# Performance work log

Measured on AMD Instinct MI355X. Metric: run time of the kernel, lower is better.

The kernel has to match this reference:

```python
import jax, jax.numpy as jnp
import numpy as np

EMBED_DIM = 1024
NUM_MEMORY_SLOTS = 256
B, Q = 8, 4096


def setup_inputs() -> dict:
    key = jax.random.key(0)
    ks = jax.random.split(key, 6)
    s = 1.0 / np.sqrt(EMBED_DIM)
    return {
        "x": jax.random.normal(ks[0], (B, Q, EMBED_DIM), dtype=jnp.float32),
        "memory_bank": jax.random.normal(ks[1], (NUM_MEMORY_SLOTS, EMBED_DIM), dtype=jnp.float32),
        "Wq": jax.random.uniform(ks[2], (EMBED_DIM, EMBED_DIM), jnp.float32, -s, s),
        "bq": jax.random.uniform(ks[3], (EMBED_DIM,), jnp.float32, -s, s),
        "Wo": jax.random.uniform(ks[4], (EMBED_DIM, EMBED_DIM), jnp.float32, -s, s),
        "bo": jax.random.uniform(ks[5], (EMBED_DIM,), jnp.float32, -s, s),
    }


def reference(x, memory_bank, Wq, bq, Wo, bo):
    # query projection: [B,Q,E]
    queries = jnp.einsum('bqe,fe->bqf', x, Wq) + bq
    # attention over fixed memory bank: scores [B,Q,M]
    scores = jnp.einsum('bqe,me->bqm', queries, memory_bank)
    weights = jax.nn.softmax(scores, axis=-1)
    attended = jnp.einsum('bqm,me->bqe', weights, memory_bank)
    # output projection + residual
    return jnp.einsum('bqe,fe->bqf', attended, Wo) + bo + x
```

## Files before the change

### kernel.cpp

```cpp
#include <hip/hip_runtime.h>
#include <hip/hip_bf16.h>
#include <stdint.h>

#define TOK 32768
#define EMB 1024
#define MSL 256

typedef __attribute__((ext_vector_type(8))) short short8;
typedef __attribute__((ext_vector_type(4))) float f32x4;

__device__ __forceinline__ ushort f2bf(float f) {
    union { float f; uint32_t u; } c; c.f = f;
    uint32_t u = c.u;
    return (ushort)((u + 0x7fffu + ((u >> 16) & 1u)) >> 16);
}

__device__ __forceinline__ void split2(float f, ushort& h, ushort& l) {
    union { float f; uint32_t u; } c; c.f = f;
    h = (ushort)(c.u >> 16);
    union { uint32_t u; float f; } hv; hv.u = c.u & 0xffff0000u;
    union { float f; uint32_t u; } lc; lc.f = f - hv.f;
    l = (ushort)(lc.u >> 16);
}

__device__ __forceinline__ void async_copy16(const void* gsrc, void* ldst) {
    __builtin_amdgcn_global_load_lds(
        (const __attribute__((address_space(1))) uint32_t*)gsrc,
        (__attribute__((address_space(3))) uint32_t*)ldst,
        16, 0, 0);
}

__global__ __launch_bounds__(256) void split_f32(const float* __restrict__ in,
                                                 ushort* __restrict__ hi,
                                                 ushort* __restrict__ lo) {
    int i = blockIdx.x * 256 + threadIdx.x;
    float4 v = ((const float4*)in)[i];
    ushort4 h4, l4;
    split2(v.x, h4.x, l4.x); split2(v.y, h4.y, l4.y);
    split2(v.z, h4.z, l4.z); split2(v.w, h4.w, l4.w);
    ((ushort4*)hi)[i] = h4;
    ((ushort4*)lo)[i] = l4;
}

__global__ __launch_bounds__(256) void transpose_split(const float* __restrict__ in,
                                                       ushort* __restrict__ outh,
                                                       ushort* __restrict__ outl) {
    __shared__ float ld[64 * 65];
    const int t = threadIdx.x;
    const int eBase = blockIdx.x * 64;
    const int fBase = blockIdx.y * 64;
    #pragma unroll
    for (int r = 0; r < 16; ++r) {
        int row = r * 4 + (t >> 6);
        int col = t & 63;
        ld[row * 65 + col] = in[(size_t)(fBase + row) * EMB + eBase + col];
    }
    __syncthreads();
    #pragma unroll
    for (int r = 0; r < 16; ++r) {
        int row = r * 4 + (t >> 6);
        int col = t & 63;
        float v = ld[col * 65 + row];
        ushort h, l; split2(v, h, l);
        size_t o = (size_t)(eBase + row) * EMB + fBase + col;
        outh[o] = h; outl[o] = l;
    }
}

__global__ __launch_bounds__(256) void dot_c(const float* __restrict__ bq,
                                             const float* __restrict__ mb,
                                             float* __restrict__ c) {
    int m = blockIdx.x * 4 + (threadIdx.x >> 6);
    int lane = threadIdx.x & 63;
    const float4* mrow = (const float4*)(mb + (size_t)m * EMB);
    const float4* brow = (const float4*)bq;
    float s = 0.f;
    #pragma unroll
    for (int k = 0; k < 4; ++k) {
        float4 a = mrow[lane + k * 64];
        float4 b = brow[lane + k * 64];
        s += a.x * b.x + a.y * b.y + a.z * b.z + a.w * b.w;
    }
    #pragma unroll
    for (int off = 32; off; off >>= 1) s += __shfl_xor(s, off, 64);
    if (lane == 0) c[m] = s;
}

__global__ __launch_bounds__(256) void softmax_rows(const float* __restrict__ scores,
                                                    ushort* __restrict__ w) {
    int row = blockIdx.x * 4 + (threadIdx.x >> 6);
    int lane = threadIdx.x & 63;
    const float4 v = ((const float4*)(scores + (size_t)row * MSL))[lane];
    float mx = fmaxf(fmaxf(v.x, v.y), fmaxf(v.z, v.w));
    #pragma unroll
    for (int off = 32; off; off >>= 1) mx = fmaxf(mx, __shfl_xor(mx, off, 64));
    float e0 = __expf(v.x - mx), e1 = __expf(v.y - mx);
    float e2 = __expf(v.z - mx), e3 = __expf(v.w - mx);
    float s = e0 + e1 + e2 + e3;
    #pragma unroll
    for (int off = 32; off; off >>= 1) s += __shfl_xor(s, off, 64);
    float inv = 1.0f / s;
    ushort4 o;
    o.x = f2bf(e0 * inv); o.y = f2bf(e1 * inv); o.z = f2bf(e2 * inv); o.w = f2bf(e3 * inv);
    ((ushort4*)(w + (size_t)row * MSL))[lane] = o;
}

template<bool ADD_BIAS, bool OUT_BF16>
__global__ __launch_bounds__(256) void gemm_s(
    const float* __restrict__ A, const ushort* __restrict__ Bh,
    const ushort* __restrict__ Bl, const float* __restrict__ bias,
    void* __restrict__ Cout, int K, int ldc)
{
    __shared__ ushort sAh[128 * 64];
    __shared__ ushort sAl[128 * 64];
    __shared__ ushort sBh[128 * 64];
    __shared__ ushort sBl[128 * 64];

    const int t = threadIdx.x;
    const int lane = t & 63;
    const int wave = t >> 6;
    const int wr = wave >> 1;
    const int wc = wave & 1;
    const int rowBase = blockIdx.y * 128;
    const int colBase = blockIdx.x * 128;

    const float*  Ab  = A  + (size_t)rowBase * K;
    const ushort* Bhb = Bh + (size_t)colBase * K;
    const ushort* Blb = Bl + (size_t)colBase * K;

    f32x4 acc[4][4] = {};

    const int kIters = K >> 6;
    for (int kt = 0; kt < kIters; ++kt) {
        const int k0 = kt << 6;
        __syncthreads();
        #pragma unroll
        for (int r = 0; r < 4; ++r) {
            int i = r * 256 + t;
            int row = i >> 3;
            int col = (i & 7) << 3;
            async_copy16(Bhb + (size_t)row * K + k0 + col, &sBh[(size_t)(r * 256 + wave * 64) * 8]);
            async_copy16(Blb + (size_t)row * K + k0 + col, &sBl[(size_t)(r * 256 + wave * 64) * 8]);
        }
        #pragma unroll
        for (int r = 0; r < 4; ++r) {
            int i = r * 256 + t;
            int row = i >> 3;
            int col = (i & 7) << 3;
            const float* src = Ab + (size_t)row * K + k0 + col;
            float4 f0 = *(const float4*)src;
            float4 f1 = *(const float4*)(src + 4);
            short8 hv, lv; ushort h, l;
            split2(f0.x, h, l); hv[0] = (short)h; lv[0] = (short)l;
            split2(f0.y, h, l); hv[1] = (short)h; lv[1] = (short)l;
            split2(f0.z, h, l); hv[2] = (short)h; lv[2] = (short)l;
            split2(f0.w, h, l); hv[3] = (short)h; lv[3] = (short)l;
            split2(f1.x, h, l); hv[4] = (short)h; lv[4] = (short)l;
            split2(f1.y, h, l); hv[5] = (short)h; lv[5] = (short)l;
            split2(f1.z, h, l); hv[6] = (short)h; lv[6] = (short)l;
            split2(f1.w, h, l); hv[7] = (short)h; lv[7] = (short)l;
            *(short8*)&sAh[(size_t)i * 8] = hv;
            *(short8*)&sAl[(size_t)i * 8] = lv;
        }
        __syncthreads();

        #pragma unroll
        for (int ks = 0; ks < 2; ++ks) {
            const int kloc = ks * 32 + (lane >> 4) * 8;
            short8 ah[4], al[4], bh[4], bl[4];
            #pragma unroll
            for (int i2 = 0; i2 < 4; ++i2) {
                int row = wr * 64 + i2 * 16 + (lane & 15);
                ah[i2] = *(const short8*)&sAh[row * 64 + kloc];
                al[i2] = *(const short8*)&sAl[row * 64 + kloc];
            }
            #pragma unroll
            for (int j = 0; j < 4; ++j) {
                int row = wc * 64 + j * 16 + (lane & 15);
                bh[j] = *(const short8*)&sBh[row * 64 + kloc];
                bl[j] = *(const short8*)&sBl[row * 64 + kloc];
            }
            #pragma unroll
            for (int i2 = 0; i2 < 4; ++i2)
                #pragma unroll
                for (int j = 0; j < 4; ++j) {
                    acc[i2][j] = __builtin_amdgcn_mfma_f32_16x16x32_bf16(ah[i2], bh[j], acc[i2][j], 0, 0, 0);
                    acc[i2][j] = __builtin_amdgcn_mfma_f32_16x16x32_bf16(ah[i2], bl[j], acc[i2][j], 0, 0, 0);
                    acc[i2][j] = __builtin_amdgcn_mfma_f32_16x16x32_bf16(al[i2], bh[j], acc[i2][j], 0, 0, 0);
                }
        }
    }

    #pragma unroll
    for (int i2 = 0; i2 < 4; ++i2) {
        #pragma unroll
        for (int j = 0; j < 4; ++j) {
            const int col = colBase + wc * 64 + j * 16 + (lane & 15);
            float bcol = ADD_BIAS ? bias[col] : 0.0f;
            #pragma unroll
            for (int r = 0; r < 4; ++r) {
                const int row = rowBase + wr * 64 + i2 * 16 + ((lane >> 4) << 2) + r;
                float v = acc[i2][j][r] + bcol;
                if (OUT_BF16)
                    ((ushort*)Cout)[(size_t)row * ldc + col] = f2bf(v);
                else
                    ((float*)Cout)[(size_t)row * ldc + col] = v;
            }
        }
    }
}

template<bool ADD_BIAS, bool ADD_RESID, bool OUT_BF16>
__global__ __launch_bounds__(256) void gemm_bt(
    const ushort* __restrict__ A, const ushort* __restrict__ Bm,
    const float* __restrict__ bias, const float* __restrict__ resid,
    void* __restrict__ Cout, int K, int ldc)
{
    __shared__ ushort sA[128 * 64];
    __shared__ ushort sB[128 * 64];

    const int t = threadIdx.x;
    const int lane = t & 63;
    const int wave = t >> 6;
    const int wr = wave >> 1;
    const int wc = wave & 1;
    const int rowBase = blockIdx.y * 128;
    const int colBase = blockIdx.x * 128;

    const ushort* Ab = A + (size_t)rowBase * K;
    const ushort* Bb = Bm + (size_t)colBase * K;

    f32x4 acc[4][4] = {};

    const int kIters = K >> 6;
    for (int kt = 0; kt < kIters; ++kt) {
        const int k0 = kt << 6;
        __syncthreads();
        #pragma unroll
        for (int r = 0; r < 4; ++r) {
            int i = r * 256 + t;
            int row = i >> 3;
            int col = (i & 7) << 3;
            async_copy16(Ab + (size_t)row * K + k0 + col, &sA[(size_t)(r * 256 + wave * 64) * 8]);
        }
        #pragma unroll
        for (int r = 0; r < 4; ++r) {
            int i = r * 256 + t;
            int row = i >> 3;
            int col = (i & 7) << 3;
            async_copy16(Bb + (size_t)row * K + k0 + col, &sB[(size_t)(r * 256 + wave * 64) * 8]);
        }
        __syncthreads();

        #pragma unroll
        for (int ks = 0; ks < 2; ++ks) {
            const int kloc = ks * 32 + (lane >> 4) * 8;
            short8 a[4], b[4];
            #pragma unroll
            for (int i2 = 0; i2 < 4; ++i2) {
                int row = wr * 64 + i2 * 16 + (lane & 15);
                a[i2] = *(const short8*)&sA[row * 64 + kloc];
            }
            #pragma unroll
            for (int j = 0; j < 4; ++j) {
                int row = wc * 64 + j * 16 + (lane & 15);
                b[j] = *(const short8*)&sB[row * 64 + kloc];
            }
            #pragma unroll
            for (int i2 = 0; i2 < 4; ++i2)
                #pragma unroll
                for (int j = 0; j < 4; ++j)
                    acc[i2][j] = __builtin_amdgcn_mfma_f32_16x16x32_bf16(
                        a[i2], b[j], acc[i2][j], 0, 0, 0);
        }
    }

    #pragma unroll
    for (int i2 = 0; i2 < 4; ++i2) {
        #pragma unroll
        for (int j = 0; j < 4; ++j) {
            const int col = colBase + wc * 64 + j * 16 + (lane & 15);
            float bcol = ADD_BIAS ? bias[col] : 0.0f;
            #pragma unroll
            for (int r = 0; r < 4; ++r) {
                const int row = rowBase + wr * 64 + i2 * 16 + ((lane >> 4) << 2) + r;
                float v = acc[i2][j][r] + bcol;
                if (ADD_RESID) v += resid[(size_t)row * ldc + col];
                if (OUT_BF16)
                    ((ushort*)Cout)[(size_t)row * ldc + col] = f2bf(v);
                else
                    ((float*)Cout)[(size_t)row * ldc + col] = v;
            }
        }
    }
}

extern "C" void kernel_launch(void* const* d_in, const int* in_sizes, int n_in,
                              void* d_out, int out_size, void* d_ws, size_t ws_size,
                              hipStream_t stream) {
    const float* x  = (const float*)d_in[0];
    const float* mb = (const float*)d_in[1];
    const float* Wq = (const float*)d_in[2];
    const float* bq = (const float*)d_in[3];
    const float* Wo = (const float*)d_in[4];
    const float* bo = (const float*)d_in[5];
    float* out = (float*)d_out;

    char* ws = (char*)d_ws;
    size_t o = 0;
    float*  sc   = (float*)(ws + o);  o += (size_t)TOK * MSL * 4;
    ushort* wgt  = (ushort*)(ws + o); o += (size_t)TOK * MSL * 2;
    ushort* mbh  = (ushort*)(ws + o); o += (size_t)MSL * EMB * 2;
    ushort* mbl  = (ushort*)(ws + o); o += (size_t)MSL * EMB * 2;
    ushort* wqth = (ushort*)(ws + o); o += (size_t)EMB * EMB * 2;
    ushort* wqtl = (ushort*)(ws + o); o += (size_t)EMB * EMB * 2;
    float*  P    = (float*)(ws + o);  o += (size_t)MSL * EMB * 4;
    ushort* Ph   = (ushort*)(ws + o); o += (size_t)MSL * EMB * 2;
    ushort* Pl   = (ushort*)(ws + o); o += (size_t)MSL * EMB * 2;
    ushort* RTb  = (ushort*)(ws + o); o += (size_t)EMB * MSL * 2;
    float*  cvec = (float*)(ws + o);  o += (size_t)MSL * 4;

    split_f32<<<(MSL * EMB / 4) / 256, 256, 0, stream>>>(mb, mbh, mbl);
    transpose_split<<<dim3(16, 16), 256, 0, stream>>>(Wq, wqth, wqtl);
    dot_c<<<MSL / 4, 256, 0, stream>>>(bq, mb, cvec);

    gemm_s<false, false><<<dim3(EMB / 128, MSL / 128), 256, 0, stream>>>(
        mb, wqth, wqtl, nullptr, P, EMB, EMB);
    split_f32<<<(MSL * EMB / 4) / 256, 256, 0, stream>>>(P, Ph, Pl);

    gemm_s<false, true><<<dim3(MSL / 128, EMB / 128), 256, 0, stream>>>(
        Wo, mbh, mbl, nullptr, RTb, EMB, MSL);

    gemm_s<true, false><<<dim3(MSL / 128, TOK / 128), 256, 0, stream>>>(
        x, Ph, Pl, cvec, sc, EMB, MSL);

    softmax_rows<<<TOK / 4, 256, 0, stream>>>(sc, wgt);

    gemm_bt<true, true, false><<<dim3(EMB / 128, TOK / 128), 256, 0, stream>>>(
        wgt, RTb, bo, x, out, MSL, EMB);
}
```

Measured before the change: 430.0 us.

## Split-K the small weight GEMMs with atomics and XOR-swizzle LDS tiles

The two small precompute GEMMs (memory_bank×Wq and Wo×memory_bank) ran on only 16 blocks each. They now use split-K over 16 z-slices, accumulating into zeroed fp32 buffers with atomicAdd, and the result is cast to bf16 afterwards. LDS tiles in both GEMM kernels also get an XOR swizzle on the 16-byte column chunk, aimed at removing bank conflicts on the MFMA operand reads. This adds a zeroing kernel, a cast kernel and atomic traffic, and the summation order becomes nondeterministic.

```diff
diff --git a/kernel.cpp b/kernel.cpp
--- a/kernel.cpp
+++ b/kernel.cpp
@@ -28,6 +28,20 @@
         (const __attribute__((address_space(1))) uint32_t*)gsrc,
         (__attribute__((address_space(3))) uint32_t*)ldst,
         16, 0, 0);
+}
+
+__global__ __launch_bounds__(256) void zero_f32(float* __restrict__ p) {
+    int i = blockIdx.x * 256 + threadIdx.x;
+    ((float4*)p)[i] = float4{0.f, 0.f, 0.f, 0.f};
+}
+
+__global__ __launch_bounds__(256) void cast_f32_bf16(const float* __restrict__ in,
+                                                     ushort* __restrict__ out) {
+    int i = blockIdx.x * 256 + threadIdx.x;
+    float4 v = ((const float4*)in)[i];
+    ushort4 o;
+    o.x = f2bf(v.x); o.y = f2bf(v.y); o.z = f2bf(v.z); o.w = f2bf(v.w);
+    ((ushort4*)out)[i] = o;
 }
 
 __global__ __launch_bounds__(256) void split_f32(const float* __restrict__ in,
@@ -105,7 +119,8 @@
     ((ushort4*)(w + (size_t)row * MSL))[lane] = o;
 }
 
-template<bool ADD_BIAS, bool OUT_BF16>
+
+template<bool ADD_BIAS, bool OUT_BF16, bool ATOMIC>
 __global__ __launch_bounds__(256) void gemm_s(
     const float* __restrict__ A, const ushort* __restrict__ Bh,
     const ushort* __restrict__ Bl, const float* __restrict__ bias,
@@ -128,26 +143,26 @@
     const ushort* Bhb = Bh + (size_t)colBase * K;
     const ushort* Blb = Bl + (size_t)colBase * K;
 
+    const int cg = ((t & 7) ^ ((t >> 3) & 7)) << 3;
+
     f32x4 acc[4][4] = {};
 
-    const int kIters = K >> 6;
-    for (int kt = 0; kt < kIters; ++kt) {
+    const int kIters = (K >> 6) / (ATOMIC ? gridDim.z : 1);
+    const int ktBase = ATOMIC ? blockIdx.z * kIters : 0;
+    for (int kt = ktBase; kt < ktBase + kIters; ++kt) {
         const int k0 = kt << 6;
         __syncthreads();
         #pragma unroll
         for (int r = 0; r < 4; ++r) {
-            int i = r * 256 + t;
-            int row = i >> 3;
-            int col = (i & 7) << 3;
-            async_copy16(Bhb + (size_t)row * K + k0 + col, &sBh[(size_t)(r * 256 + wave * 64) * 8]);
-            async_copy16(Blb + (size_t)row * K + k0 + col, &sBl[(size_t)(r * 256 + wave * 64) * 8]);
+            int row = r * 32 + (t >> 3);
+            async_copy16(Bhb + (size_t)row * K + k0 + cg, &sBh[(size_t)(r * 256 + wave * 64) * 8]);
+            async_copy16(Blb + (size_t)row * K + k0 + cg, &sBl[(size_t)(r * 256 + wave * 64) * 8]);
         }
         #pragma unroll
         for (int r = 0; r < 4; ++r) {
             int i = r * 256 + t;
-            int row = i >> 3;
-            int col = (i & 7) << 3;
-            const float* src = Ab + (size_t)row * K + k0 + col;
+            int row = r * 32 + (t >> 3);
+            const float* src = Ab + (size_t)row * K + k0 + cg;
             float4 f0 = *(const float4*)src;
             float4 f1 = *(const float4*)(src + 4);
             short8 hv, lv; ushort h, l;
@@ -166,19 +181,21 @@
 
         #pragma unroll
         for (int ks = 0; ks < 2; ++ks) {
-            const int kloc = ks * 32 + (lane >> 4) * 8;
+            const int kc = ks * 4 + (lane >> 4);
             short8 ah[4], al[4], bh[4], bl[4];
             #pragma unroll
             for (int i2 = 0; i2 < 4; ++i2) {
                 int row = wr * 64 + i2 * 16 + (lane & 15);
-                ah[i2] = *(const short8*)&sAh[row * 64 + kloc];
-                al[i2] = *(const short8*)&sAl[row * 64 + kloc];
+                int off = row * 64 + ((kc ^ (row & 7)) << 3);
+                ah[i2] = *(const short8*)&sAh[off];
+                al[i2] = *(const short8*)&sAl[off];
             }
             #pragma unroll
             for (int j = 0; j < 4; ++j) {
                 int row = wc * 64 + j * 16 + (lane & 15);
-                bh[j] = *(const short8*)&sBh[row * 64 + kloc];
-                bl[j] = *(const short8*)&sBl[row * 64 + kloc];
+                int off = row * 64 + ((kc ^ (row & 7)) << 3);
+                bh[j] = *(const short8*)&sBh[off];
+                bl[j] = *(const short8*)&sBl[off];
             }
             #pragma unroll
             for (int i2 = 0; i2 < 4; ++i2)
@@ -201,7 +218,9 @@
             for (int r = 0; r < 4; ++r) {
                 const int row = rowBase + wr * 64 + i2 * 16 + ((lane >> 4) << 2) + r;
                 float v = acc[i2][j][r] + bcol;
-                if (OUT_BF16)
+                if (ATOMIC)
+                    atomicAdd(&((float*)Cout)[(size_t)row * ldc + col], v);
+                else if (OUT_BF16)
                     ((ushort*)Cout)[(size_t)row * ldc + col] = f2bf(v);
                 else
                     ((float*)Cout)[(size_t)row * ldc + col] = v;
@@ -230,6 +249,8 @@
     const ushort* Ab = A + (size_t)rowBase * K;
     const ushort* Bb = Bm + (size_t)colBase * K;
 
+    const int cg = ((t & 7) ^ ((t >> 3) & 7)) << 3;
+
     f32x4 acc[4][4] = {};
 
     const int kIters = K >> 6;
@@ -238,33 +259,25 @@
         __syncthreads();
         #pragma unroll
         for (int r = 0; r < 4; ++r) {
-            int i = r * 256 + t;
-            int row = i >> 3;
-            int col = (i & 7) << 3;
-            async_copy16(Ab + (size_t)row * K + k0 + col, &sA[(size_t)(r * 256 + wave * 64) * 8]);
-        }
-        #pragma unroll
-        for (int r = 0; r < 4; ++r) {
-            int i = r * 256 + t;
-            int row = i >> 3;
-            int col = (i & 7) << 3;
-            async_copy16(Bb + (size_t)row * K + k0 + col, &sB[(size_t)(r * 256 + wave * 64) * 8]);
+            int row = r * 32 + (t >> 3);
+            async_copy16(Ab + (size_t)row * K + k0 + cg, &sA[(size_t)(r * 256 + wave * 64) * 8]);
+            async_copy16(Bb + (size_t)row * K + k0 + cg, &sB[(size_t)(r * 256 + wave * 64) * 8]);
         }
         __syncthreads();
 
         #pragma unroll
         for (int ks = 0; ks < 2; ++ks) {
-            const int kloc = ks * 32 + (lane >> 4) * 8;
+            const int kc = ks * 4 + (lane >> 4);
             short8 a[4], b[4];
             #pragma unroll
             for (int i2 = 0; i2 < 4; ++i2) {
                 int row = wr * 64 + i2 * 16 + (lane & 15);
-                a[i2] = *(const short8*)&sA[row * 64 + kloc];
+                a[i2] = *(const short8*)&sA[row * 64 + ((kc ^ (row & 7)) << 3)];
             }
             #pragma unroll
             for (int j = 0; j < 4; ++j) {
                 int row = wc * 64 + j * 16 + (lane & 15);
-                b[j] = *(const short8*)&sB[row * 64 + kloc];
+                b[j] = *(const short8*)&sB[row * 64 + ((kc ^ (row & 7)) << 3)];
             }
             #pragma unroll
             for (int i2 = 0; i2 < 4; ++i2)
@@ -308,30 +321,34 @@
 
     char* ws = (char*)d_ws;
     size_t o = 0;
+    float*  P    = (float*)(ws + o);  o += (size_t)MSL * EMB * 4;
+    float*  RTf  = (float*)(ws + o);  o += (size_t)EMB * MSL * 4;
     float*  sc   = (float*)(ws + o);  o += (size_t)TOK * MSL * 4;
     ushort* wgt  = (ushort*)(ws + o); o += (size_t)TOK * MSL * 2;
     ushort* mbh  = (ushort*)(ws + o); o += (size_t)MSL * EMB * 2;
     ushort* mbl  = (ushort*)(ws + o); o += (size_t)MSL * EMB * 2;
     ushort* wqth = (ushort*)(ws + o); o += (size_t)EMB * EMB * 2;
     ushort* wqtl = (ushort*)(ws + o); o += (size_t)EMB * EMB * 2;
-    float*  P    = (float*)(ws + o);  o += (size_t)MSL * EMB * 4;
     ushort* Ph   = (ushort*)(ws + o); o += (size_t)MSL * EMB * 2;
     ushort* Pl   = (ushort*)(ws + o); o += (size_t)MSL * EMB * 2;
     ushort* RTb  = (ushort*)(ws + o); o += (size_t)EMB * MSL * 2;
     float*  cvec = (float*)(ws + o);  o += (size_t)MSL * 4;
 
+    zero_f32<<<(2 * MSL * EMB / 4) / 256, 256, 0, stream>>>(P);
+
     split_f32<<<(MSL * EMB / 4) / 256, 256, 0, stream>>>(mb, mbh, mbl);
     transpose_split<<<dim3(16, 16), 256, 0, stream>>>(Wq, wqth, wqtl);
     dot_c<<<MSL / 4, 256, 0, stream>>>(bq, mb, cvec);
 
-    gemm_s<false, false><<<dim3(EMB / 128, MSL / 128), 256, 0, stream>>>(
+    gemm_s<false, false, true><<<dim3(EMB / 128, MSL / 128, 16), 256, 0, stream>>>(
         mb, wqth, wqtl, nullptr, P, EMB, EMB);
     split_f32<<<(MSL * EMB / 4) / 256, 256, 0, stream>>>(P, Ph, Pl);
 
-    gemm_s<false, true><<<dim3(MSL / 128, EMB / 128), 256, 0, stream>>>(
-        Wo, mbh, mbl, nullptr, RTb, EMB, MSL);
-
-    gemm_s<true, false><<<dim3(MSL / 128, TOK / 128), 256, 0, stream>>>(
+    gemm_s<false, false, true><<<dim3(MSL / 128, EMB / 128, 16), 256, 0, stream>>>(
+        Wo, mbh, mbl, nullptr, RTf, EMB, MSL);
+    cast_f32_bf16<<<(EMB * MSL / 4) / 256, 256, 0, stream>>>(RTf, RTb);
+
+    gemm_s<true, false, false><<<dim3(MSL / 128, TOK / 128, 1), 256, 0, stream>>>(
         x, Ph, Pl, cvec, sc, EMB, MSL);
 
     softmax_rows<<<TOK / 4, 256, 0, stream>>>(sc, wgt);
```

After: 374.0 us. -13.0%, faster.
